# Optimization experiments

Hardware: AMD Instinct MI355X
Metric: run time of the kernel (lower is better)

The kernel has to match this reference:

```python
import jax, jax.numpy as jnp
import numpy as np

B, D, K, L, H = 16384, 1024, 512, 128, 64  # batch, input_dim, num_components, latent_dim, phi hidden
EPS = 1e-9


def setup_inputs() -> dict:
    key = jax.random.key(0)
    k0, k1, k2, k3 = jax.random.split(key, 4)
    # small scales keep squared distances O(1-10) so exp(-d2) is non-degenerate
    x = jax.random.normal(k0, (B, D), jnp.float32) * 0.03
    z_samples = jax.random.normal(k1, (K, L), jnp.float32)
    W1 = jax.random.normal(k2, (L, H), jnp.float32) * (1.0 / np.sqrt(L)).astype(np.float32)
    b1 = jnp.zeros((H,), jnp.float32)
    W2 = jax.random.normal(k3, (H, D), jnp.float32) * 0.01
    b2 = jnp.zeros((D,), jnp.float32)
    return {"x": x, "z_samples": z_samples, "W1": W1, "b1": b1, "W2": W2, "b2": b2}


def reference(x, z_samples, W1, b1, W2, b2):
    # PhiNet: Linear -> ReLU -> Linear, applied to all components at once
    phi = jnp.maximum(z_samples @ W1 + b1, 0.0) @ W2 + b2          # (K, D)
    # ||x - phi_k||^2 for all (k, b) via GEMM expansion (fuses the per-component loop)
    sq = (jnp.sum(phi * phi, axis=-1)[:, None]
          + jnp.sum(x * x, axis=-1)[None, :]
          - 2.0 * (phi @ x.T))                                      # (K, B)
    lik = jnp.exp(-sq)                                              # (K, B)
    # weights = 1/K; sum_k w * lik = mean over K
    mixture_ll = jnp.log(jnp.mean(lik, axis=0) + EPS)               # (B,)
    return mixture_ll.mean()
```

## Files before the change

### kernel.cpp

```cpp
#include <hip/hip_runtime.h>
#include <hip/hip_bf16.h>
#include <stdint.h>

#define N_B   16384
#define D_DIM 1024
#define K_K   512
#define L_DIM 128
#define H_DIM 64

typedef __attribute__((ext_vector_type(8))) short short8;
typedef __attribute__((ext_vector_type(4))) float f32x4;

__device__ __forceinline__ unsigned short f2bf(float f) {
    union { float f; unsigned int u; } c; c.f = f;
    unsigned int u = c.u;
    unsigned int r = (u + 0x7FFFu + ((u >> 16) & 1u)) >> 16;
    return (unsigned short)r;
}

__device__ __forceinline__ unsigned int pk2(float a, float b) {
    __hip_bfloat162 t = __float22bfloat162_rn(make_float2(a, b));
    union { __hip_bfloat162 h; unsigned int u; } c; c.h = t;
    return c.u;
}

__global__ __launch_bounds__(256) void prep_kernel(
    const float* __restrict__ z, const float* __restrict__ W1,
    const float* __restrict__ b1, const float* __restrict__ W2,
    const float* __restrict__ b2, unsigned short* __restrict__ W2bf,
    unsigned short* __restrict__ h_bf, float* __restrict__ phi2) {
    __shared__ float zsh[8][L_DIM];
    __shared__ float hsh[8][H_DIM];
    __shared__ float redp[4][8];
    const int tid = threadIdx.x;
    const int k0 = blockIdx.x * 8;

    {
        int i = blockIdx.x * 256 + tid;
        float4 v = ((const float4*)W2)[i];
        uint2 o = make_uint2(pk2(v.x, v.y), pk2(v.z, v.w));
        *(uint2*)(W2bf + i * 4) = o;
    }
#pragma unroll
    for (int c = 0; c < 4; ++c) {
        int idx = c * 256 + tid;
        zsh[idx >> 7][idx & 127] = z[k0 * L_DIM + idx];
    }
    __syncthreads();
    {
        const int j = tid & 63, kk = tid >> 6;
        float bb = b1[j];
        float s0 = bb, s1 = bb;
        for (int l = 0; l < L_DIM; ++l) {
            float w = W1[l * H_DIM + j];
            s0 += zsh[kk][l] * w;
            s1 += zsh[kk + 4][l] * w;
        }
        float h0 = fmaxf(s0, 0.0f), h1 = fmaxf(s1, 0.0f);
        hsh[kk][j] = h0; hsh[kk + 4][j] = h1;
        h_bf[(k0 + kk) * H_DIM + j]     = f2bf(h0);
        h_bf[(k0 + kk + 4) * H_DIM + j] = f2bf(h1);
    }
    __syncthreads();
    float ss[8] = {0.f, 0.f, 0.f, 0.f, 0.f, 0.f, 0.f, 0.f};
#pragma unroll
    for (int c = 0; c < 4; ++c) {
        int d = c * 256 + tid;
        float bb = b2[d];
        float a[8];
#pragma unroll
        for (int kk = 0; kk < 8; ++kk) a[kk] = bb;
        for (int j = 0; j < H_DIM; ++j) {
            float w = W2[j * D_DIM + d];
#pragma unroll
            for (int kk = 0; kk < 8; ++kk) a[kk] += hsh[kk][j] * w;
        }
#pragma unroll
        for (int kk = 0; kk < 8; ++kk) ss[kk] += a[kk] * a[kk];
    }
    const int lane = tid & 63, wv = tid >> 6;
#pragma unroll
    for (int kk = 0; kk < 8; ++kk) {
        float v = ss[kk];
#pragma unroll
        for (int o = 1; o < 64; o <<= 1) v += __shfl_xor(v, o, 64);
        if (lane == 0) redp[wv][kk] = v;
    }
    __syncthreads();
    if (tid < 8) phi2[k0 + tid] = redp[0][tid] + redp[1][tid] + redp[2][tid] + redp[3][tid];
}

__global__ __launch_bounds__(256) void main_kernel(
    const float* __restrict__ x, const unsigned short* __restrict__ W2bf,
    const unsigned short* __restrict__ h_bf, const float* __restrict__ phi2,
    const float* __restrict__ b2, float* __restrict__ out) {
    __shared__ float upart[4][32][68];
    __shared__ __align__(16) unsigned short u_tile[32 * 72];
    __shared__ float phi2s[K_K];
    __shared__ __align__(16) float b2l[D_DIM];
    __shared__ float x2p4[4][32], xb2p4[4][32];
    __shared__ float red[4][32];

    const int tid = threadIdx.x;
    const int wv  = tid >> 6;
    const int l   = tid & 63;
    const int lm  = l & 15;
    const int q   = l >> 4;
    const int n0  = blockIdx.x * 32;
    const int dq  = wv * 256;

    float4 xv[2][8][2];
#pragma unroll
    for (int i = 0; i < 2; ++i) {
        const float* xp = x + (size_t)(n0 + i * 16 + lm) * D_DIM + dq + q * 8;
#pragma unroll
        for (int s = 0; s < 8; ++s) {
            xv[i][s][0] = *(const float4*)(xp + s * 32);
            xv[i][s][1] = *(const float4*)(xp + s * 32 + 4);
        }
    }
    phi2s[tid]       = phi2[tid];
    phi2s[256 + tid] = phi2[256 + tid];
    ((float4*)b2l)[tid] = ((const float4*)b2)[tid];
    __syncthreads();

    short8 wf[2][4];
#pragma unroll
    for (int j = 0; j < 4; ++j)
        wf[0][j] = *(const short8*)(W2bf + (size_t)(j * 16 + lm) * D_DIM + dq + q * 8);

    f32x4 c1[2][4] = {};
    float x2p0 = 0.f, x2p1 = 0.f, xbp0 = 0.f, xbp1 = 0.f;
#pragma unroll
    for (int s = 0; s < 8; ++s) {
        const int cur = s & 1, nxt = cur ^ 1;
        if (s < 7) {
#pragma unroll
            for (int j = 0; j < 4; ++j)
                wf[nxt][j] = *(const short8*)(W2bf + (size_t)(j * 16 + lm) * D_DIM + dq + (s + 1) * 32 + q * 8);
        }
        const int dl = dq + s * 32 + q * 8;
        float4 bb0 = *(const float4*)&b2l[dl];
        float4 bb1 = *(const float4*)&b2l[dl + 4];
        short8 af[2];
#pragma unroll
        for (int i = 0; i < 2; ++i) {
            float4 v0 = xv[i][s][0], v1 = xv[i][s][1];
            float s2 = v0.x*v0.x + v0.y*v0.y + v0.z*v0.z + v0.w*v0.w
                     + v1.x*v1.x + v1.y*v1.y + v1.z*v1.z + v1.w*v1.w;
            float sb = v0.x*bb0.x + v0.y*bb0.y + v0.z*bb0.z + v0.w*bb0.w
                     + v1.x*bb1.x + v1.y*bb1.y + v1.z*bb1.z + v1.w*bb1.w;
            union { short8 s8; unsigned int u[4]; } packu;
            packu.u[0] = pk2(v0.x, v0.y);
            packu.u[1] = pk2(v0.z, v0.w);
            packu.u[2] = pk2(v1.x, v1.y);
            packu.u[3] = pk2(v1.z, v1.w);
            af[i] = packu.s8;
            if (i == 0) { x2p0 += s2; xbp0 += sb; } else { x2p1 += s2; xbp1 += sb; }
        }
#pragma unroll
        for (int i = 0; i < 2; ++i)
#pragma unroll
            for (int j = 0; j < 4; ++j)
                c1[i][j] = __builtin_amdgcn_mfma_f32_16x16x32_bf16(af[i], wf[cur][j], c1[i][j], 0, 0, 0);
    }
#pragma unroll
    for (int i = 0; i < 2; ++i)
#pragma unroll
        for (int j = 0; j < 4; ++j)
#pragma unroll
            for (int r = 0; r < 4; ++r)
                upart[wv][i * 16 + q * 4 + r][j * 16 + lm] = c1[i][j][r];
    x2p0 += __shfl_xor(x2p0, 16, 64); x2p0 += __shfl_xor(x2p0, 32, 64);
    x2p1 += __shfl_xor(x2p1, 16, 64); x2p1 += __shfl_xor(x2p1, 32, 64);
    xbp0 += __shfl_xor(xbp0, 16, 64); xbp0 += __shfl_xor(xbp0, 32, 64);
    xbp1 += __shfl_xor(xbp1, 16, 64); xbp1 += __shfl_xor(xbp1, 32, 64);
    if (l < 16) {
        x2p4[wv][l] = x2p0;  x2p4[wv][16 + l] = x2p1;
        xb2p4[wv][l] = xbp0; xb2p4[wv][16 + l] = xbp1;
    }
    __syncthreads();
#pragma unroll
    for (int c = 0; c < 8; ++c) {
        int idx = c * 256 + tid;
        int row = idx >> 6, col = idx & 63;
        float sum = upart[0][row][col] + upart[1][row][col]
                  + upart[2][row][col] + upart[3][row][col];
        u_tile[row * 72 + col] = f2bf(sum);
    }
    __syncthreads();

    f32x4 acc[8][2] = {};
#pragma unroll
    for (int ks = 0; ks < 2; ++ks) {
        const int ko = ks * 32 + q * 8;
        short8 bfr[2];
#pragma unroll
        for (int j = 0; j < 2; ++j)
            bfr[j] = *(const short8*)&u_tile[(j * 16 + lm) * 72 + ko];
#pragma unroll
        for (int i = 0; i < 8; ++i) {
            short8 a = *(const short8*)(h_bf + (size_t)(wv * 128 + i * 16 + lm) * H_DIM + ko);
#pragma unroll
            for (int j = 0; j < 2; ++j)
                acc[i][j] = __builtin_amdgcn_mfma_f32_16x16x32_bf16(a, bfr[j], acc[i][j], 0, 0, 0);
        }
    }
    float xn0 = (x2p4[0][lm] + x2p4[1][lm] + x2p4[2][lm] + x2p4[3][lm])
        - 2.f * (xb2p4[0][lm] + xb2p4[1][lm] + xb2p4[2][lm] + xb2p4[3][lm]);
    float xn1 = (x2p4[0][16 + lm] + x2p4[1][16 + lm] + x2p4[2][16 + lm] + x2p4[3][16 + lm])
        - 2.f * (xb2p4[0][16 + lm] + xb2p4[1][16 + lm] + xb2p4[2][16 + lm] + xb2p4[3][16 + lm]);
    float cs0 = 0.f, cs1 = 0.f;
#pragma unroll
    for (int i = 0; i < 8; ++i) {
#pragma unroll
        for (int r = 0; r < 4; ++r) {
            float p2 = phi2s[wv * 128 + i * 16 + q * 4 + r];
            cs0 += __expf(-(p2 + xn0 - 2.f * acc[i][0][r]));
            cs1 += __expf(-(p2 + xn1 - 2.f * acc[i][1][r]));
        }
    }
    cs0 += __shfl_xor(cs0, 16, 64); cs0 += __shfl_xor(cs0, 32, 64);
    cs1 += __shfl_xor(cs1, 16, 64); cs1 += __shfl_xor(cs1, 32, 64);
    if (l < 16) { red[wv][l] = cs0; red[wv][16 + l] = cs1; }
    __syncthreads();
    if (tid < 32) {
        float row_lik = red[0][tid] + red[1][tid] + red[2][tid] + red[3][tid];
        float lg = __logf(row_lik * (1.0f / (float)K_K) + 1e-9f);
        lg += __shfl_xor(lg, 1, 64);
        lg += __shfl_xor(lg, 2, 64);
        lg += __shfl_xor(lg, 4, 64);
        lg += __shfl_xor(lg, 8, 64);
        lg += __shfl_xor(lg, 16, 64);
        if (tid == 0) atomicAdd(out, lg * (1.0f / (float)N_B));
    }
}

extern "C" void kernel_launch(void* const* d_in, const int* in_sizes, int n_in,
                              void* d_out, int out_size, void* d_ws, size_t ws_size,
                              hipStream_t stream) {
    const float* x  = (const float*)d_in[0];
    const float* z  = (const float*)d_in[1];
    const float* W1 = (const float*)d_in[2];
    const float* b1 = (const float*)d_in[3];
    const float* W2 = (const float*)d_in[4];
    const float* b2 = (const float*)d_in[5];

    char* ws = (char*)d_ws;
    unsigned short* W2bf = (unsigned short*)(ws);
    unsigned short* h_bf = (unsigned short*)(ws + 131072);
    float*          phi2 = (float*)(ws + 196608);

    hipMemsetAsync(d_out, 0, sizeof(float), stream);
    prep_kernel<<<64, 256, 0, stream>>>(z, W1, b1, W2, b2, W2bf, h_bf, phi2);
    main_kernel<<<N_B / 32, 256, 0, stream>>>(x, W2bf, h_bf, phi2, b2, (float*)d_out);
}
```

Baseline: 150.0 us.

## Stagger x column loads per block, shrink register buffer, reduce partials via LDS atomics

Cuts the per-thread x register buffer from all 8 column slices down to a 4-slot ring that is refilled during the loop. Each block starts at a different column chunk (phase = blockIdx & 7), which spreads concurrent global accesses. The cross-wave reduction of the first GEMM moves from a 4-way partial-sum LDS array plus a separate reduce pass to LDS float atomicAdd into a single tile, and bf16 packing now happens when fragments are read. This lowers register and LDS use and removes one barrier, at the cost of atomic contention and the loss of W2 double-buffering.

New measurement: 164.7 us. 1.1x slower.

```diff
diff --git a/kernel.cpp b/kernel.cpp
--- a/kernel.cpp
+++ b/kernel.cpp
@@ -94,11 +94,10 @@
     const float* __restrict__ x, const unsigned short* __restrict__ W2bf,
     const unsigned short* __restrict__ h_bf, const float* __restrict__ phi2,
     const float* __restrict__ b2, float* __restrict__ out) {
-    __shared__ float upart[4][32][68];
-    __shared__ __align__(16) unsigned short u_tile[32 * 72];
+    __shared__ float u32s[32][64];
     __shared__ float phi2s[K_K];
     __shared__ __align__(16) float b2l[D_DIM];
-    __shared__ float x2p4[4][32], xb2p4[4][32];
+    __shared__ float x2s[32], xb2s[32];
     __shared__ float red[4][32];
 
     const int tid = threadIdx.x;
@@ -108,44 +107,46 @@
     const int q   = l >> 4;
     const int n0  = blockIdx.x * 32;
     const int dq  = wv * 256;
-
-    float4 xv[2][8][2];
-#pragma unroll
-    for (int i = 0; i < 2; ++i) {
-        const float* xp = x + (size_t)(n0 + i * 16 + lm) * D_DIM + dq + q * 8;
-#pragma unroll
-        for (int s = 0; s < 8; ++s) {
-            xv[i][s][0] = *(const float4*)(xp + s * 32);
-            xv[i][s][1] = *(const float4*)(xp + s * 32 + 4);
-        }
-    }
+    const int phase = blockIdx.x & 7;
+
+    ((float4*)u32s)[tid]       = make_float4(0.f, 0.f, 0.f, 0.f);
+    ((float4*)u32s)[256 + tid] = make_float4(0.f, 0.f, 0.f, 0.f);
+    if (tid < 32) { x2s[tid] = 0.f; xb2s[tid] = 0.f; }
     phi2s[tid]       = phi2[tid];
     phi2s[256 + tid] = phi2[256 + tid];
     ((float4*)b2l)[tid] = ((const float4*)b2)[tid];
     __syncthreads();
 
-    short8 wf[2][4];
-#pragma unroll
-    for (int j = 0; j < 4; ++j)
-        wf[0][j] = *(const short8*)(W2bf + (size_t)(j * 16 + lm) * D_DIM + dq + q * 8);
+    float4 xv[4][2][2];
+#pragma unroll
+    for (int p = 0; p < 4; ++p) {
+        const int cc = (p + phase) & 7;
+        const int dcol = dq + cc * 32 + q * 8;
+#pragma unroll
+        for (int i = 0; i < 2; ++i) {
+            const float* xp = x + (size_t)(n0 + i * 16 + lm) * D_DIM + dcol;
+            xv[p][i][0] = *(const float4*)xp;
+            xv[p][i][1] = *(const float4*)(xp + 4);
+        }
+    }
 
     f32x4 c1[2][4] = {};
     float x2p0 = 0.f, x2p1 = 0.f, xbp0 = 0.f, xbp1 = 0.f;
 #pragma unroll
-    for (int s = 0; s < 8; ++s) {
-        const int cur = s & 1, nxt = cur ^ 1;
-        if (s < 7) {
-#pragma unroll
-            for (int j = 0; j < 4; ++j)
-                wf[nxt][j] = *(const short8*)(W2bf + (size_t)(j * 16 + lm) * D_DIM + dq + (s + 1) * 32 + q * 8);
-        }
-        const int dl = dq + s * 32 + q * 8;
-        float4 bb0 = *(const float4*)&b2l[dl];
-        float4 bb1 = *(const float4*)&b2l[dl + 4];
+    for (int c = 0; c < 8; ++c) {
+        const int rg = c & 3;
+        const int cc = (c + phase) & 7;
+        const int dcol = dq + cc * 32 + q * 8;
+        short8 wf[4];
+#pragma unroll
+        for (int j = 0; j < 4; ++j)
+            wf[j] = *(const short8*)(W2bf + (size_t)(j * 16 + lm) * D_DIM + dcol);
+        float4 bb0 = *(const float4*)&b2l[dcol];
+        float4 bb1 = *(const float4*)&b2l[dcol + 4];
         short8 af[2];
 #pragma unroll
         for (int i = 0; i < 2; ++i) {
-            float4 v0 = xv[i][s][0], v1 = xv[i][s][1];
+            float4 v0 = xv[rg][i][0], v1 = xv[rg][i][1];
             float s2 = v0.x*v0.x + v0.y*v0.y + v0.z*v0.z + v0.w*v0.w
                      + v1.x*v1.x + v1.y*v1.y + v1.z*v1.z + v1.w*v1.w;
             float sb = v0.x*bb0.x + v0.y*bb0.y + v0.z*bb0.z + v0.w*bb0.w
@@ -158,11 +159,21 @@
             af[i] = packu.s8;
             if (i == 0) { x2p0 += s2; xbp0 += sb; } else { x2p1 += s2; xbp1 += sb; }
         }
+        if (c < 4) {
+            const int cc2 = (c + 4 + phase) & 7;
+            const int dcol2 = dq + cc2 * 32 + q * 8;
+#pragma unroll
+            for (int i = 0; i < 2; ++i) {
+                const float* xp = x + (size_t)(n0 + i * 16 + lm) * D_DIM + dcol2;
+                xv[rg][i][0] = *(const float4*)xp;
+                xv[rg][i][1] = *(const float4*)(xp + 4);
+            }
+        }
 #pragma unroll
         for (int i = 0; i < 2; ++i)
 #pragma unroll
             for (int j = 0; j < 4; ++j)
-                c1[i][j] = __builtin_amdgcn_mfma_f32_16x16x32_bf16(af[i], wf[cur][j], c1[i][j], 0, 0, 0);
+                c1[i][j] = __builtin_amdgcn_mfma_f32_16x16x32_bf16(af[i], wf[j], c1[i][j], 0, 0, 0);
     }
 #pragma unroll
     for (int i = 0; i < 2; ++i)
@@ -170,23 +181,14 @@
         for (int j = 0; j < 4; ++j)
 #pragma unroll
             for (int r = 0; r < 4; ++r)
-                upart[wv][i * 16 + q * 4 + r][j * 16 + lm] = c1[i][j][r];
+                atomicAdd(&u32s[i * 16 + q * 4 + r][j * 16 + lm], c1[i][j][r]);
     x2p0 += __shfl_xor(x2p0, 16, 64); x2p0 += __shfl_xor(x2p0, 32, 64);
     x2p1 += __shfl_xor(x2p1, 16, 64); x2p1 += __shfl_xor(x2p1, 32, 64);
     xbp0 += __shfl_xor(xbp0, 16, 64); xbp0 += __shfl_xor(xbp0, 32, 64);
     xbp1 += __shfl_xor(xbp1, 16, 64); xbp1 += __shfl_xor(xbp1, 32, 64);
     if (l < 16) {
-        x2p4[wv][l] = x2p0;  x2p4[wv][16 + l] = x2p1;
-        xb2p4[wv][l] = xbp0; xb2p4[wv][16 + l] = xbp1;
-    }
-    __syncthreads();
-#pragma unroll
-    for (int c = 0; c < 8; ++c) {
-        int idx = c * 256 + tid;
-        int row = idx >> 6, col = idx & 63;
-        float sum = upart[0][row][col] + upart[1][row][col]
-                  + upart[2][row][col] + upart[3][row][col];
-        u_tile[row * 72 + col] = f2bf(sum);
+        atomicAdd(&x2s[l], x2p0);       atomicAdd(&x2s[16 + l], x2p1);
+        atomicAdd(&xb2s[l], xbp0);      atomicAdd(&xb2s[16 + l], xbp1);
     }
     __syncthreads();
 
@@ -196,8 +198,16 @@
         const int ko = ks * 32 + q * 8;
         short8 bfr[2];
 #pragma unroll
-        for (int j = 0; j < 2; ++j)
-            bfr[j] = *(const short8*)&u_tile[(j * 16 + lm) * 72 + ko];
+        for (int j = 0; j < 2; ++j) {
+            float4 p0 = *(const float4*)&u32s[j * 16 + lm][ko];
+            float4 p1 = *(const float4*)&u32s[j * 16 + lm][ko + 4];
+            union { short8 s8; unsigned int u[4]; } pb;
+            pb.u[0] = pk2(p0.x, p0.y);
+            pb.u[1] = pk2(p0.z, p0.w);
+            pb.u[2] = pk2(p1.x, p1.y);
+            pb.u[3] = pk2(p1.z, p1.w);
+            bfr[j] = pb.s8;
+        }
 #pragma unroll
         for (int i = 0; i < 8; ++i) {
             short8 a = *(const short8*)(h_bf + (size_t)(wv * 128 + i * 16 + lm) * H_DIM + ko);
@@ -206,10 +216,8 @@
                 acc[i][j] = __builtin_amdgcn_mfma_f32_16x16x32_bf16(a, bfr[j], acc[i][j], 0, 0, 0);
         }
     }
-    float xn0 = (x2p4[0][lm] + x2p4[1][lm] + x2p4[2][lm] + x2p4[3][lm])
-        - 2.f * (xb2p4[0][lm] + xb2p4[1][lm] + xb2p4[2][lm] + xb2p4[3][lm]);
-    float xn1 = (x2p4[0][16 + lm] + x2p4[1][16 + lm] + x2p4[2][16 + lm] + x2p4[3][16 + lm])
-        - 2.f * (xb2p4[0][16 + lm] + xb2p4[1][16 + lm] + xb2p4[2][16 + lm] + xb2p4[3][16 + lm]);
+    float xn0 = x2s[lm]      - 2.f * xb2s[lm];
+    float xn1 = x2s[16 + lm] - 2.f * xb2s[16 + lm];
     float cs0 = 0.f, cs1 = 0.f;
 #pragma unroll
     for (int i = 0; i < 8; ++i) {
```
